# Optimization experiments

Hardware: AMD Instinct MI355X
Metric: run time of the kernel (lower is better)

Reference implementation:

```python
import jax, jax.numpy as jnp
import numpy as np
from jax import lax

B, S, V, E, H, L, LAT = 32, 64, 32000, 128, 512, 2, 64

def setup_inputs() -> dict:
    key = jax.random.key(0)
    ks = jax.random.split(key, 40)
    sc = 0.05
    inputs = jax.random.randint(ks[0], (B, S), 0, V, dtype=jnp.int32)
    lengths = jnp.sort(jax.random.randint(ks[1], (B,), 1, S + 1, dtype=jnp.int32))[::-1]
    lengths = lengths.at[0].set(S)  # enforce_sorted=True, max length == S for static shapes
    d = {
        'inputs': inputs,
        'lengths': lengths,
        'noise': jax.random.normal(ks[2], (L, B, LAT), jnp.float32),
        'embed_table': jax.random.normal(ks[3], (V, E), jnp.float32) * sc,
        'enc_Wm': jax.random.normal(ks[4], (LAT, E), jnp.float32) * sc,
        'enc_bm': jnp.zeros((LAT,), jnp.float32),
        'enc_Wv': jax.random.normal(ks[5], (LAT, E), jnp.float32) * sc,
        'enc_bv': jnp.zeros((LAT,), jnp.float32),
        'W_l2r': jax.random.normal(ks[6], (H, LAT), jnp.float32) * sc,
        'b_l2r': jnp.zeros((H,), jnp.float32),
        'gru_Wih0': jax.random.normal(ks[7], (3 * H, E), jnp.float32) * sc,
        'gru_Whh0': jax.random.normal(ks[8], (3 * H, H), jnp.float32) * sc,
        'gru_bih0': jnp.zeros((3 * H,), jnp.float32),
        'gru_bhh0': jnp.zeros((3 * H,), jnp.float32),
        'gru_Wih1': jax.random.normal(ks[9], (3 * H, H), jnp.float32) * sc,
        'gru_Whh1': jax.random.normal(ks[10], (3 * H, H), jnp.float32) * sc,
        'gru_bih1': jnp.zeros((3 * H,), jnp.float32),
        'gru_bhh1': jnp.zeros((3 * H,), jnp.float32),
        'W_out': jax.random.normal(ks[11], (V, H), jnp.float32) * sc,
        'b_out': jnp.zeros((V,), jnp.float32),
        'logp_W1': jax.random.normal(ks[12], (200, LAT), jnp.float32) * sc,
        'logp_b1': jnp.zeros((200,), jnp.float32),
        'logp_W2': jax.random.normal(ks[13], (100, 200), jnp.float32) * sc,
        'logp_b2': jnp.zeros((100,), jnp.float32),
        'logp_W3': jax.random.normal(ks[14], (1, 100), jnp.float32) * sc,
        'logp_b3': jnp.zeros((1,), jnp.float32),
        'sas_W1': jax.random.normal(ks[15], (200, LAT), jnp.float32) * sc,
        'sas_b1': jnp.zeros((200,), jnp.float32),
        'sas_W2': jax.random.normal(ks[16], (100, 200), jnp.float32) * sc,
        'sas_b2': jnp.zeros((100,), jnp.float32),
        'sas_W3': jax.random.normal(ks[17], (1, 100), jnp.float32) * sc,
        'sas_b3': jnp.zeros((1,), jnp.float32),
    }
    return d

def _gru_layer(x, h0, Wih, Whh, bih, bhh, lengths):
    # x: [B,T,D]; PyTorch GRU gate order: r, z, n. Packed semantics: state frozen
    # and output zero beyond each sample's length.
    T = x.shape[1]
    xW = jnp.einsum('btd,gd->btg', x, Wih) + bih          # [B,T,3H] one big GEMM
    tmask = jnp.arange(T)[:, None] < lengths[None, :]      # [T,B]
    def step(h, inp):
        xw_t, m_t = inp                                    # [B,3H], [B]
        hW = h @ Whh.T + bhh
        xr, xz, xn = jnp.split(xw_t, 3, axis=-1)
        hr, hz, hn = jnp.split(hW, 3, axis=-1)
        r = jax.nn.sigmoid(xr + hr)
        u = jax.nn.sigmoid(xz + hz)
        n = jnp.tanh(xn + r * hn)
        h_new = (1.0 - u) * n + u * h
        m = m_t[:, None]
        h = jnp.where(m, h_new, h)
        out = jnp.where(m, h_new, 0.0)
        return h, out
    hT, outs = lax.scan(step, h0, (xW.transpose(1, 0, 2), tmask))
    return outs.transpose(1, 0, 2), hT                     # [B,T,H], [B,H]

def _mlp3(x, W1, b1, W2, b2, W3, b3):
    h = jax.nn.relu(x @ W1.T + b1)
    h = jax.nn.relu(h @ W2.T + b2)
    return (h @ W3.T + b3).reshape(-1)

def reference(inputs, lengths, noise, embed_table, enc_Wm, enc_bm, enc_Wv, enc_bv,
              W_l2r, b_l2r, gru_Wih0, gru_Whh0, gru_bih0, gru_bhh0,
              gru_Wih1, gru_Whh1, gru_bih1, gru_bhh1, W_out, b_out,
              logp_W1, logp_b1, logp_W2, logp_b2, logp_W3, logp_b3,
              sas_W1, sas_b1, sas_W2, sas_b2, sas_W3, sas_b3):
    emb = embed_table[inputs]                              # [B,S,E] gather
    # ragged masked segment-sum: sum embeddings of tokens with id > 2 per sample
    mask = (inputs > 2)[..., None].astype(emb.dtype)
    vec_frag = jnp.sum(emb * mask, axis=1)                 # [B,E]
    mean = vec_frag @ enc_Wm.T + enc_bm                    # [B,LAT]
    logv = vec_frag @ enc_Wv.T + enc_bv
    std = jnp.exp(0.5 * logv)
    z = noise * std + mean                                 # [L,B,LAT]
    pred_logp = _mlp3(mean, logp_W1, logp_b1, logp_W2, logp_b2, logp_W3, logp_b3)
    pred_sas = _mlp3(mean, sas_W1, sas_b1, sas_W2, sas_b2, sas_W3, sas_b3)
    state = z @ W_l2r.T + b_l2r                            # [L,B,H]
    # decoder: 2-layer GRU (eval mode: no dropout), then vocab projection
    out0, _ = _gru_layer(emb, state[0], gru_Wih0, gru_Whh0, gru_bih0, gru_bhh0, lengths)
    out1, _ = _gru_layer(out0, state[1], gru_Wih1, gru_Whh1, gru_bih1, gru_bhh1, lengths)
    output = out1 @ W_out.T + b_out                        # [B,S,V]
    return (output, mean, std, z, pred_logp, pred_sas)
```

## Files before the change

### kernel.cpp

```cpp
#include <hip/hip_runtime.h>


typedef __attribute__((ext_vector_type(8))) short bf16x8_t;
typedef __attribute__((ext_vector_type(8))) unsigned short u16x8_t;
typedef __attribute__((ext_vector_type(4))) float f32x4_t;
typedef __attribute__((ext_vector_type(8))) _Float16 f16x8_t;
typedef __attribute__((ext_vector_type(4))) unsigned int u32x4_t;

#define AS_AGENT __HIP_MEMORY_SCOPE_AGENT

static __device__ __forceinline__ unsigned short f2bf(float f) {
    unsigned int u = __float_as_uint(f);
    u += 0x7fffu + ((u >> 16) & 1u);
    return (unsigned short)(u >> 16);
}
static __device__ __forceinline__ unsigned short bfround(unsigned int u) {
    u += 0x7fffu + ((u >> 16) & 1u);
    return (unsigned short)(u >> 16);
}
static __device__ __forceinline__ unsigned short f2h(float f) {
    _Float16 h = (_Float16)f;
    return __builtin_bit_cast(unsigned short, h);
}
static __device__ __forceinline__ float sigmoidf_(float x) {
    return 1.f / (1.f + __expf(-x));
}

__global__ __launch_bounds__(256) void embed_encoder_kernel(
    const int* __restrict__ tok, const float* __restrict__ table,
    const float* __restrict__ Wih0f,
    const float* __restrict__ Wm, const float* __restrict__ bm,
    const float* __restrict__ Wv, const float* __restrict__ bv,
    const float* __restrict__ noise,
    const float* __restrict__ Wl2r, const float* __restrict__ bl2r,
    const float* __restrict__ lW1, const float* __restrict__ lb1,
    const float* __restrict__ lW2, const float* __restrict__ lb2,
    const float* __restrict__ lW3, const float* __restrict__ lb3,
    const float* __restrict__ sW1, const float* __restrict__ sb1,
    const float* __restrict__ sW2, const float* __restrict__ sb2,
    const float* __restrict__ sW3, const float* __restrict__ sb3,
    float* __restrict__ o_mean, float* __restrict__ o_std, float* __restrict__ o_z,
    float* __restrict__ o_logp, float* __restrict__ o_sas,
    float* __restrict__ state,
    unsigned short* __restrict__ embb,
    unsigned short* __restrict__ Wih0b)
{
    const int b = blockIdx.x, tid = threadIdx.x;
    __shared__ float v_[128], mn[64], sd[64], zz[2][64], hh1[200], hh2[100];
    if (tid < 128) {
        const int e = tid;
        float acc = 0.f;
        for (int s = 0; s < 64; ++s) {
            int id = tok[b * 64 + s];
            float v = table[(size_t)id * 128 + e];
            embb[(size_t)(b * 64 + s) * 128 + e] = f2bf(v);
            if (id > 2) acc += v;
        }
        v_[e] = acc;
    }
    for (int i = b * 256 + tid; i < 49152; i += 8192) {
        float4 v = reinterpret_cast<const float4*>(Wih0f)[i];
        ushort4 o;
        o.x = f2bf(v.x); o.y = f2bf(v.y); o.z = f2bf(v.z); o.w = f2bf(v.w);
        reinterpret_cast<ushort4*>(Wih0b)[i] = o;
    }
    __syncthreads();
    if (tid < 128) {
        int j = tid & 63;
        bool isv = tid >= 64;
        const float* W = (isv ? Wv : Wm) + j * 128;
        float a = isv ? bv[j] : bm[j];
#pragma unroll 4
        for (int k = 0; k < 128; ++k) a = fmaf(v_[k], W[k], a);
        if (!isv) { mn[j] = a; o_mean[b * 64 + j] = a; }
        else      { float s = __expf(0.5f * a); sd[j] = s; o_std[b * 64 + j] = s; }
    }
    __syncthreads();
    if (tid < 128) {
        int l = tid >> 6, j = tid & 63;
        float zv = fmaf(noise[(l * 32 + b) * 64 + j], sd[j], mn[j]);
        zz[l][j] = zv;
        o_z[(l * 32 + b) * 64 + j] = zv;
    }
    __syncthreads();
#pragma unroll
    for (int p = 0; p < 4; ++p) {
        int tt = p * 256 + tid;
        int l = tt >> 9, hd = tt & 511;
        const float* W = Wl2r + hd * 64;
        float a = bl2r[hd];
#pragma unroll 4
        for (int k = 0; k < 64; ++k) a = fmaf(zz[l][k], W[k], a);
        state[(size_t)(l * 32 + b) * 512 + hd] = a;
    }
    if (tid < 200) {
        const float* W = lW1 + tid * 64;
        float a = lb1[tid];
        for (int k = 0; k < 64; ++k) a = fmaf(mn[k], W[k], a);
        hh1[tid] = fmaxf(a, 0.f);
    }
    __syncthreads();
    if (tid < 100) {
        const float* W = lW2 + tid * 200;
        float a = lb2[tid];
        for (int k = 0; k < 200; ++k) a = fmaf(hh1[k], W[k], a);
        hh2[tid] = fmaxf(a, 0.f);
    }
    __syncthreads();
    if (tid == 0) {
        float a = lb3[0];
        for (int k = 0; k < 100; ++k) a = fmaf(hh2[k], lW3[k], a);
        o_logp[b] = a;
    }
    __syncthreads();
    if (tid < 200) {
        const float* W = sW1 + tid * 64;
        float a = sb1[tid];
        for (int k = 0; k < 64; ++k) a = fmaf(mn[k], W[k], a);
        hh1[tid] = fmaxf(a, 0.f);
    }
    __syncthreads();
    if (tid < 100) {
        const float* W = sW2 + tid * 200;
        float a = sb2[tid];
        for (int k = 0; k < 200; ++k) a = fmaf(hh1[k], W[k], a);
        hh2[tid] = fmaxf(a, 0.f);
    }
    __syncthreads();
    if (tid == 0) {
        float a = sb3[0];
        for (int k = 0; k < 100; ++k) a = fmaf(hh2[k], sW3[k], a);
        o_sas[b] = a;
    }
}

__global__ __launch_bounds__(256) void gemm_bt_kernel(
    const unsigned short* __restrict__ A,
    const unsigned short* __restrict__ B,
    const float* __restrict__ bias,
    float* __restrict__ C,
    int M, int N, int K)
{
    __shared__ unsigned short lA[128 * 64];
    __shared__ unsigned short lB[128 * 64];
    const int tid = threadIdx.x;
    const int lane = tid & 63;
    const int wave = tid >> 6;
    const int wm = wave >> 1, wn = wave & 1;
    const int m0 = blockIdx.y * 128, n0 = blockIdx.x * 128;

    f32x4_t acc[4][4];
#pragma unroll
    for (int i = 0; i < 4; ++i)
#pragma unroll
        for (int j = 0; j < 4; ++j) acc[i][j] = (f32x4_t){0.f, 0.f, 0.f, 0.f};

    for (int kt = 0; kt < K; kt += 64) {
#pragma unroll
        for (int p = 0; p < 4; ++p) {
            int g = p * 256 + tid;
            int row = g >> 3, c8 = g & 7;
            int dst = row * 64 + ((c8 ^ (row & 7)) << 3);
            *(u16x8_t*)&lA[dst] = *(const u16x8_t*)(A + (size_t)(m0 + row) * K + kt + (c8 << 3));
            *(u16x8_t*)&lB[dst] = *(const u16x8_t*)(B + (size_t)(n0 + row) * K + kt + (c8 << 3));
        }
        __syncthreads();
#pragma unroll
        for (int kc = 0; kc < 2; ++kc) {
            bf16x8_t af[4], bfr[4];
            int c8 = kc * 4 + (lane >> 4);
#pragma unroll
            for (int i = 0; i < 4; ++i) {
                int ra = wm * 64 + i * 16 + (lane & 15);
                af[i] = *(const bf16x8_t*)&lA[ra * 64 + ((c8 ^ (ra & 7)) << 3)];
                int rb = wn * 64 + i * 16 + (lane & 15);
                bfr[i] = *(const bf16x8_t*)&lB[rb * 64 + ((c8 ^ (rb & 7)) << 3)];
            }
#pragma unroll
            for (int i = 0; i < 4; ++i)
#pragma unroll
                for (int j = 0; j < 4; ++j)
                    acc[i][j] = __builtin_amdgcn_mfma_f32_16x16x32_bf16(af[i], bfr[j], acc[i][j], 0, 0, 0);
        }
        __syncthreads();
    }
    const int lm = (lane >> 4) * 4, ln = lane & 15;
#pragma unroll
    for (int i = 0; i < 4; ++i) {
        int gm = m0 + wm * 64 + i * 16 + lm;
#pragma unroll
        for (int j = 0; j < 4; ++j) {
            int gn = n0 + wn * 64 + j * 16 + ln;
            float bb = bias ? bias[gn] : 0.f;
#pragma unroll
            for (int r = 0; r < 4; ++r)
                C[(size_t)(gm + r) * N + gn] = acc[i][j][r] + bb;
        }
    }
}

#define NWG_L0 16
#define NWG_TOT 48
#define NWG_ALL 256
#define NWG_GEMM 208
#define OCH 32832

__global__ __launch_bounds__(512) void gru_fused_kernel(
    const float* __restrict__ xW0,
    const float* __restrict__ Whh0, const float* __restrict__ bhh0,
    const float* __restrict__ Whh1, const float* __restrict__ Wih1,
    const float* __restrict__ bih1, const float* __restrict__ bhh1,
    const float* __restrict__ hinit,
    const int* __restrict__ lengths,
    unsigned short* __restrict__ h0x,
    unsigned short* __restrict__ h1x,
    unsigned short* __restrict__ o0x,
    unsigned short* __restrict__ out1x,
    const float* __restrict__ Woutf,
    unsigned short* __restrict__ Woutb,
    const float* __restrict__ bout,
    float* __restrict__ outp,
    int* __restrict__ flags)
{
    __shared__ __align__(16) char smem[157184];
    const int tid = threadIdx.x;
    const int wg = blockIdx.x;
    const int lane = tid & 63;
    const int wave = tid >> 6;
    unsigned int* __restrict__ h0x32 = (unsigned int*)h0x;
    unsigned int* __restrict__ h1x32 = (unsigned int*)h1x;
    unsigned int* __restrict__ o0x32 = (unsigned int*)o0x;
    unsigned int* __restrict__ o1x32 = (unsigned int*)out1x;

    (void)__hip_atomic_load(&flags[0], __ATOMIC_ACQUIRE, AS_AGENT);

    if (wg >= NWG_TOT) {
        unsigned short* lA = (unsigned short*)smem;
        unsigned short* lB = (unsigned short*)(smem + 16384);
        const int g = wg - NWG_TOT;
        const int wm = wave >> 2;
        const int wn = wave & 3;

        for (int pn = g; pn < 250; pn += NWG_GEMM) {
            const u32x4_t* src = (const u32x4_t*)Woutf + (size_t)pn * 16384;
            unsigned long long* dst = (unsigned long long*)Woutb + (size_t)pn * 16384;
            for (int i = tid; i < 16384; i += 512) {
                u32x4_t q = __builtin_nontemporal_load(src + i);
                unsigned int lo = (unsigned int)bfround(q[0]) | ((unsigned int)bfround(q[1]) << 16);
                unsigned int hi = (unsigned int)bfround(q[2]) | ((unsigned int)bfround(q[3]) << 16);
                unsigned long long w = (unsigned long long)lo | ((unsigned long long)hi << 32);
                __hip_atomic_store(dst + i, w, __ATOMIC_RELAXED, AS_AGENT);
            }
            asm volatile("s_waitcnt vmcnt(0)" ::: "memory");
            __syncthreads();
            if (tid == 0)
                __hip_atomic_store(&flags[2048 + pn * 16], 1, __ATOMIC_RELAXED, AS_AGENT);
        }

        int mPrev = -1;
        for (int T = g; T < 4000; T += NWG_GEMM) {
            const int m = T / 250, n = T % 250;
            if (m != mPrev) {
                if (wave == 0) {
                    const int tgt = 4 * m + 6;
                    for (;;) {
                        int v = 0x40000000;
                        if (lane < 32)
                            v = __hip_atomic_load(&flags[(NWG_L0 + lane) << 5],
                                                  __ATOMIC_RELAXED, AS_AGENT);
                        if (__all(v >= tgt)) break;
                        __builtin_amdgcn_s_sleep(8);
                    }
                }
                mPrev = m;
            }
            if (wave == 0) {
                while (__hip_atomic_load(&flags[2048 + n * 16], __ATOMIC_RELAXED, AS_AGENT) < 1)
                    __builtin_amdgcn_s_sleep(8);
            }
            __syncthreads();

            f32x4_t acc[4][2];
#pragma unroll
            for (int i = 0; i < 4; ++i)
#pragma unroll
                for (int j = 0; j < 2; ++j) acc[i][j] = (f32x4_t){0.f, 0.f, 0.f, 0.f};

            for (int kt = 0; kt < 512; kt += 64) {
#pragma unroll
                for (int p = 0; p < 2; ++p) {
                    int gi = p * 512 + tid;
                    int row = gi >> 3, c8 = gi & 7;
                    int dst = row * 64 + ((c8 ^ (row & 7)) << 3);
                    u32x4_t qa = *(const u32x4_t*)(out1x + (size_t)m * 65664 +
                                                   row * 512 + kt + (c8 << 3));
                    u32x4_t qb = *(const u32x4_t*)(Woutb + ((size_t)(n * 128 + row)) * 512 +
                                                   kt + (c8 << 3));
                    *(u32x4_t*)&lA[dst] = qa;
                    *(u32x4_t*)&lB[dst] = qb;
                }
                __syncthreads();
#pragma unroll
                for (int kc = 0; kc < 2; ++kc) {
                    bf16x8_t af[4], bfr[2];
                    int c8 = kc * 4 + (lane >> 4);
#pragma unroll
                    for (int i = 0; i < 4; ++i) {
                        int ra = wm * 64 + i * 16 + (lane & 15);
                        af[i] = *(const bf16x8_t*)&lA[ra * 64 + ((c8 ^ (ra & 7)) << 3)];
                    }
#pragma unroll
                    for (int j = 0; j < 2; ++j) {
                        int rb = wn * 32 + j * 16 + (lane & 15);
                        bfr[j] = *(const bf16x8_t*)&lB[rb * 64 + ((c8 ^ (rb & 7)) << 3)];
                    }
#pragma unroll
                    for (int i = 0; i < 4; ++i)
#pragma unroll
                        for (int j = 0; j < 2; ++j)
                            acc[i][j] = __builtin_amdgcn_mfma_f32_16x16x32_bf16(
                                af[i], bfr[j], acc[i][j], 0, 0, 0);
                }
                __syncthreads();
            }
            const int lm = (lane >> 4) * 4, ln = lane & 15;
#pragma unroll
            for (int i = 0; i < 4; ++i) {
                int rl0 = wm * 64 + i * 16 + lm;
#pragma unroll
                for (int j = 0; j < 2; ++j) {
                    int gn = n * 128 + wn * 32 + j * 16 + ln;
                    float bb = bout[gn];
#pragma unroll
                    for (int r = 0; r < 4; ++r) {
                        int rl = rl0 + r;
                        int t = 4 * m + (rl >> 5), b = rl & 31;
                        __builtin_nontemporal_store(acc[i][j][r] + bb,
                            &outp[(size_t)(b * 64 + t) * 32000 + gn]);
                    }
                }
            }
        }
        return;
    }

    unsigned short* Wl = (unsigned short*)smem;
    u32x4_t* hstage4 = (u32x4_t*)(smem + 98304);
    float* csm = (float*)(smem + 131072);
#define CSM(p, gt, b, c) csm[((((p)*3 + (gt)) * 32 + (b)) * 34) + (c)]
    const int gate = wave >> 1;
    const int mt = wave & 1;

    if (wg < NWG_L0) {
        const int d0 = wg * 32;
        for (int idx = tid; idx < 6144; idx += 512) {
            int ln = idx & 63, kk = (idx >> 6) & 15, nt = (idx >> 10) & 1, g_ = idx >> 11;
            int grow = g_ * 512 + d0 + nt * 16 + (ln & 15);
            int k = kk * 32 + ((ln >> 4) << 3);
            const float* src = Whh0 + (size_t)grow * 512 + k;
            f16x8_t v;
#pragma unroll
            for (int j = 0; j < 8; ++j) v[j] = (_Float16)src[j];
            *(f16x8_t*)&Wl[idx << 3] = v;
        }
        const int ub = tid >> 4, dpl = (tid & 15) * 2, ud = d0 + dpl;
        float h_lo = hinit[(size_t)ub * 512 + ud];
        float h_hi = hinit[(size_t)ub * 512 + ud + 1];
        const float br_lo = bhh0[ud],        br_hi = bhh0[ud + 1];
        const float bz_lo = bhh0[512 + ud],  bz_hi = bhh0[512 + ud + 1];
        const float bn_lo = bhh0[1024 + ud], bn_hi = bhh0[1024 + ud + 1];
        const int lenb = lengths[ub];
        {
            unsigned int hw = (unsigned int)f2h(h_lo) | ((unsigned int)f2h(h_hi) << 16);
            __hip_atomic_store(&h0x32[ub * 256 + (ud >> 1)], hw, __ATOMIC_RELAXED, AS_AGENT);
        }
        asm volatile("s_waitcnt vmcnt(0)" ::: "memory");
        __syncthreads();
        if (tid == 0) __hip_atomic_store(&flags[wg << 5], 1, __ATOMIC_RELAXED, AS_AGENT);
        const float* xrow = xW0 + (size_t)(ub * 64) * 1536 + ud;
        float2 px_r = *(const float2*)(xrow);
        float2 px_z = *(const float2*)(xrow + 512);
        float2 px_n = *(const float2*)(xrow + 1024);

        for (int r = 0; r < 64; ++r) {
            if (wave == 0) {
                for (;;) {
                    int v = 0x40000000;
                    int tgt = (lane < NWG_L0) ? (r + 1) : (r - 2);
                    if (lane < NWG_TOT)
                        v = __hip_atomic_load(&flags[lane << 5], __ATOMIC_RELAXED, AS_AGENT);
                    else
                        tgt = 0;
                    if (__all(v >= tgt)) break;
                    __builtin_amdgcn_s_sleep(1);
                }
            }
            __syncthreads();
            {
                const char* srcb = (const char*)h0x + ((r & 1) << 15);
                u32x4_t q0, q1, q2, q3;
                asm volatile("global_load_dwordx4 %0, %1, off sc0 sc1"
                             : "=v"(q0) : "v"(srcb + ((size_t)tid << 4)) : "memory");
                asm volatile("global_load_dwordx4 %0, %1, off sc0 sc1"
                             : "=v"(q1) : "v"(srcb + ((size_t)(512 + tid) << 4)) : "memory");
                asm volatile("global_load_dwordx4 %0, %1, off sc0 sc1"
                             : "=v"(q2) : "v"(srcb + ((size_t)(1024 + tid) << 4)) : "memory");
                asm volatile("global_load_dwordx4 %0, %1, off sc0 sc1"
                             : "=v"(q3) : "v"(srcb + ((size_t)(1536 + tid) << 4)) : "memory");
                asm volatile("s_waitcnt vmcnt(0)" ::: "memory");
                int g0 = tid, g1 = 512 + tid, g2 = 1024 + tid, g3 = 1536 + tid;
                hstage4[g0 ^ ((g0 >> 6) & 7)] = q0;
                hstage4[g1 ^ ((g1 >> 6) & 7)] = q1;
                hstage4[g2 ^ ((g2 >> 6) & 7)] = q2;
                hstage4[g3 ^ ((g3 >> 6) & 7)] = q3;
            }
            __syncthreads();
            if (wave < 6) {
                const int brow = mt * 16 + (lane & 15);
                const int ko = lane >> 4;
                f32x4_t acc0 = (f32x4_t){0.f, 0.f, 0.f, 0.f};
                f32x4_t acc1 = (f32x4_t){0.f, 0.f, 0.f, 0.f};
#pragma unroll
                for (int kk = 0; kk < 16; ++kk) {
                    int gg = brow * 64 + kk * 4 + ko;
                    f16x8_t af = __builtin_bit_cast(f16x8_t, hstage4[gg ^ (brow & 7)]);
                    f16x8_t bf0 = *(const f16x8_t*)&Wl[(((gate * 2 + 0) * 16 + kk) * 64 + lane) << 3];
                    f16x8_t bf1 = *(const f16x8_t*)&Wl[(((gate * 2 + 1) * 16 + kk) * 64 + lane) << 3];
                    acc0 = __builtin_amdgcn_mfma_f32_16x16x32_f16(af, bf0, acc0, 0, 0, 0);
                    acc1 = __builtin_amdgcn_mfma_f32_16x16x32_f16(af, bf1, acc1, 0, 0, 0);
                }
                const int crow = mt * 16 + ((lane >> 4) << 2), ccol = lane & 15;
#pragma unroll
                for (int rr = 0; rr < 4; ++rr) {
                    CSM(0, gate, crow + rr, ccol) = acc0[rr];
                    CSM(0, gate, crow + rr, 16 + ccol) = acc1[rr];
                }
            }
            __syncthreads();
            unsigned int ow = 0u;
            if (r < lenb) {
                float hr_lo = CSM(0, 0, ub, dpl), hr_hi = CSM(0, 0, ub, dpl + 1);
                float hz_lo = CSM(0, 1, ub, dpl), hz_hi = CSM(0, 1, ub, dpl + 1);
                float hn_lo = CSM(0, 2, ub, dpl), hn_hi = CSM(0, 2, ub, dpl + 1);
                float r0 = sigmoidf_(px_r.x + hr_lo + br_lo);
                float r1 = sigmoidf_(px_r.y + hr_hi + br_hi);
                float u0 = sigmoidf_(px_z.x + hz_lo + bz_lo);
                float u1 = sigmoidf_(px_z.y + hz_hi + bz_hi);
                float n0 = tanhf(px_n.x + r0 * (hn_lo + bn_lo));
                float n1 = tanhf(px_n.y + r1 * (hn_hi + bn_hi));
                h_lo = (1.f - u0) * n0 + u0 * h_lo;
                h_hi = (1.f - u1) * n1 + u1 * h_hi;
                ow = (unsigned int)f2h(h_lo) | ((unsigned int)f2h(h_hi) << 16);
            }
            {
                unsigned int hw = (unsigned int)f2h(h_lo) | ((unsigned int)f2h(h_hi) << 16);
                __hip_atomic_store(&h0x32[((r + 1) & 1) * 8192 + ub * 256 + (ud >> 1)],
                                   hw, __ATOMIC_RELAXED, AS_AGENT);
                __hip_atomic_store(&o0x32[(r & 3) * 8192 + ub * 256 + (ud >> 1)],
                                   ow, __ATOMIC_RELAXED, AS_AGENT);
            }
            asm volatile("s_waitcnt vmcnt(0)" ::: "memory");
            __syncthreads();
            if (tid == 0) __hip_atomic_store(&flags[wg << 5], r + 2, __ATOMIC_RELAXED, AS_AGENT);
            {
                int tn = r + 1 < 64 ? r + 1 : 63;
                const float* xp = xW0 + (size_t)(ub * 64 + tn) * 1536 + ud;
                px_r = *(const float2*)(xp);
                px_z = *(const float2*)(xp + 512);
                px_n = *(const float2*)(xp + 1024);
            }
        }
    } else {
        const int lid = wg - NWG_L0;
        const int d0 = lid * 16;
        for (int idx = tid; idx < 6144; idx += 512) {
            int ln = idx & 63, kk = (idx >> 6) & 31, g_ = idx >> 11;
            int grow = g_ * 512 + d0 + (ln & 15);
            int k = (kk & 15) * 32 + ((ln >> 4) << 3);
            const float* src = (kk < 16 ? Whh1 : Wih1) + (size_t)grow * 512 + k;
            f16x8_t v;
#pragma unroll
            for (int j = 0; j < 8; ++j) v[j] = (_Float16)src[j];
            *(f16x8_t*)&Wl[idx << 3] = v;
        }
        const bool upd = (tid < 256);
        const int ub = tid >> 3, dpl = (tid & 7) * 2, ud = d0 + dpl;
        float h_lo = 0.f, h_hi = 0.f;
        float br_lo = 0.f, br_hi = 0.f, bz_lo = 0.f, bz_hi = 0.f;
        float bxn_lo = 0.f, bxn_hi = 0.f, bhn_lo = 0.f, bhn_hi = 0.f;
        int lenb = 0;
        if (upd) {
            h_lo = hinit[16384 + (size_t)ub * 512 + ud];
            h_hi = hinit[16384 + (size_t)ub * 512 + ud + 1];
            br_lo = bih1[ud] + bhh1[ud];
            br_hi = bih1[ud + 1] + bhh1[ud + 1];
            bz_lo = bih1[512 + ud] + bhh1[512 + ud];
            bz_hi = bih1[512 + ud + 1] + bhh1[512 + ud + 1];
            bxn_lo = bih1[1024 + ud];   bxn_hi = bih1[1024 + ud + 1];
            bhn_lo = bhh1[1024 + ud];   bhn_hi = bhh1[1024 + ud + 1];
            lenb = lengths[ub];
            unsigned int hw = (unsigned int)f2h(h_lo) | ((unsigned int)f2h(h_hi) << 16);
            __hip_atomic_store(&h1x32[8192 + ub * 256 + (ud >> 1)], hw, __ATOMIC_RELAXED, AS_AGENT);
        }
        asm volatile("s_waitcnt vmcnt(0)" ::: "memory");
        __syncthreads();
        if (tid == 0) __hip_atomic_store(&flags[wg << 5], 2, __ATOMIC_RELAXED, AS_AGENT);

        for (int r = 1; r <= 64; ++r) {
            const int t1 = r - 1;
            if (wave == 0) {
                const int tgt = r + 1;
                for (;;) {
                    int v = 0x40000000;
                    if (lane < NWG_TOT)
                        v = __hip_atomic_load(&flags[lane << 5], __ATOMIC_RELAXED, AS_AGENT);
                    if (__all(v >= tgt)) break;
                    __builtin_amdgcn_s_sleep(1);
                }
            }
            __syncthreads();
            u32x4_t a0, a1, a2, a3, b0, b1, b2, b3;
            {
                const char* sh = (const char*)h1x + ((r & 1) << 15);
                const char* so = (const char*)o0x + ((t1 & 3) << 15);
                asm volatile("global_load_dwordx4 %0, %1, off sc0 sc1"
                             : "=v"(a0) : "v"(sh + ((size_t)tid << 4)) : "memory");
                asm volatile("global_load_dwordx4 %0, %1, off sc0 sc1"
                             : "=v"(a1) : "v"(sh + ((size_t)(512 + tid) << 4)) : "memory");
                asm volatile("global_load_dwordx4 %0, %1, off sc0 sc1"
                             : "=v"(a2) : "v"(sh + ((size_t)(1024 + tid) << 4)) : "memory");
                asm volatile("global_load_dwordx4 %0, %1, off sc0 sc1"
                             : "=v"(a3) : "v"(sh + ((size_t)(1536 + tid) << 4)) : "memory");
                asm volatile("global_load_dwordx4 %0, %1, off sc0 sc1"
                             : "=v"(b0) : "v"(so + ((size_t)tid << 4)) : "memory");
                asm volatile("global_load_dwordx4 %0, %1, off sc0 sc1"
                             : "=v"(b1) : "v"(so + ((size_t)(512 + tid) << 4)) : "memory");
                asm volatile("global_load_dwordx4 %0, %1, off sc0 sc1"
                             : "=v"(b2) : "v"(so + ((size_t)(1024 + tid) << 4)) : "memory");
                asm volatile("global_load_dwordx4 %0, %1, off sc0 sc1"
                             : "=v"(b3) : "v"(so + ((size_t)(1536 + tid) << 4)) : "memory");
                asm volatile("s_waitcnt vmcnt(4)" ::: "memory");
                int g0 = tid, g1 = 512 + tid, g2 = 1024 + tid, g3 = 1536 + tid;
                hstage4[g0 ^ ((g0 >> 6) & 7)] = a0;
                hstage4[g1 ^ ((g1 >> 6) & 7)] = a1;
                hstage4[g2 ^ ((g2 >> 6) & 7)] = a2;
                hstage4[g3 ^ ((g3 >> 6) & 7)] = a3;
            }
            __syncthreads();
            f32x4_t acc_h = (f32x4_t){0.f, 0.f, 0.f, 0.f};
            const int brow = mt * 16 + (lane & 15);
            const int ko = lane >> 4;
            if (wave < 6) {
#pragma unroll
                for (int kk = 0; kk < 16; ++kk) {
                    int gg = brow * 64 + kk * 4 + ko;
                    f16x8_t af = __builtin_bit_cast(f16x8_t, hstage4[gg ^ (brow & 7)]);
                    f16x8_t bf = *(const f16x8_t*)&Wl[(((gate * 32 + kk) * 64 + lane)) << 3];
                    acc_h = __builtin_amdgcn_mfma_f32_16x16x32_f16(af, bf, acc_h, 0, 0, 0);
                }
            }
            __syncthreads();
            {
                asm volatile("s_waitcnt vmcnt(0)" ::: "memory");
                int g0 = tid, g1 = 512 + tid, g2 = 1024 + tid, g3 = 1536 + tid;
                hstage4[g0 ^ ((g0 >> 6) & 7)] = b0;
                hstage4[g1 ^ ((g1 >> 6) & 7)] = b1;
                hstage4[g2 ^ ((g2 >> 6) & 7)] = b2;
                hstage4[g3 ^ ((g3 >> 6) & 7)] = b3;
            }
            __syncthreads();
            if (wave < 6) {
                f32x4_t acc_x = (f32x4_t){0.f, 0.f, 0.f, 0.f};
#pragma unroll
                for (int kk = 0; kk < 16; ++kk) {
                    int gg = brow * 64 + kk * 4 + ko;
                    f16x8_t af = __builtin_bit_cast(f16x8_t, hstage4[gg ^ (brow & 7)]);
                    f16x8_t bf = *(const f16x8_t*)&Wl[(((gate * 32 + 16 + kk) * 64 + lane)) << 3];
                    acc_x = __builtin_amdgcn_mfma_f32_16x16x32_f16(af, bf, acc_x, 0, 0, 0);
                }
                const int crow = mt * 16 + ((lane >> 4) << 2), ccol = lane & 15;
#pragma unroll
                for (int rr = 0; rr < 4; ++rr) {
                    CSM(0, gate, crow + rr, ccol) = acc_h[rr];
                    CSM(1, gate, crow + rr, ccol) = acc_x[rr];
                }
            }
            __syncthreads();
            unsigned int ow = 0u;
            if (upd) {
                if (t1 < lenb) {
                    float hr_lo = CSM(0, 0, ub, dpl), hr_hi = CSM(0, 0, ub, dpl + 1);
                    float hz_lo = CSM(0, 1, ub, dpl), hz_hi = CSM(0, 1, ub, dpl + 1);
                    float hn_lo = CSM(0, 2, ub, dpl), hn_hi = CSM(0, 2, ub, dpl + 1);
                    float xr_lo = CSM(1, 0, ub, dpl), xr_hi = CSM(1, 0, ub, dpl + 1);
                    float xz_lo = CSM(1, 1, ub, dpl), xz_hi = CSM(1, 1, ub, dpl + 1);
                    float xn_lo = CSM(1, 2, ub, dpl), xn_hi = CSM(1, 2, ub, dpl + 1);
                    float r0 = sigmoidf_(xr_lo + hr_lo + br_lo);
                    float r1 = sigmoidf_(xr_hi + hr_hi + br_hi);
                    float u0 = sigmoidf_(xz_lo + hz_lo + bz_lo);
                    float u1 = sigmoidf_(xz_hi + hz_hi + bz_hi);
                    float n0 = tanhf(xn_lo + bxn_lo + r0 * (hn_lo + bhn_lo));
                    float n1 = tanhf(xn_hi + bxn_hi + r1 * (hn_hi + bhn_hi));
                    h_lo = (1.f - u0) * n0 + u0 * h_lo;
                    h_hi = (1.f - u1) * n1 + u1 * h_hi;
                    ow = (unsigned int)f2bf(h_lo) | ((unsigned int)f2bf(h_hi) << 16);
                }
                if (r < 64) {
                    unsigned int hw = (unsigned int)f2h(h_lo) | ((unsigned int)f2h(h_hi) << 16);
                    __hip_atomic_store(&h1x32[((r + 1) & 1) * 8192 + ub * 256 + (ud >> 1)],
                                       hw, __ATOMIC_RELAXED, AS_AGENT);
                }
                __hip_atomic_store(&o1x32[(size_t)(t1 >> 2) * OCH +
                                          ((t1 & 3) * 32 + ub) * 256 + (ud >> 1)],
                                   ow, __ATOMIC_RELAXED, AS_AGENT);
            }
            asm volatile("s_waitcnt vmcnt(0)" ::: "memory");
            __syncthreads();
            if (tid == 0)
                __hip_atomic_store(&flags[wg << 5], r + 2, __ATOMIC_RELAXED, AS_AGENT);
        }
    }
#undef CSM
}

extern "C" void kernel_launch(void* const* d_in, const int* in_sizes, int n_in,
                              void* d_out, int out_size, void* d_ws, size_t ws_size,
                              hipStream_t stream) {
    const int*   tok    = (const int*)d_in[0];
    const int*   lens   = (const int*)d_in[1];
    const float* noise  = (const float*)d_in[2];
    const float* table  = (const float*)d_in[3];
    const float* Wm     = (const float*)d_in[4];
    const float* bm_    = (const float*)d_in[5];
    const float* Wv     = (const float*)d_in[6];
    const float* bv_    = (const float*)d_in[7];
    const float* Wl2r   = (const float*)d_in[8];
    const float* bl2r   = (const float*)d_in[9];
    const float* Wih0   = (const float*)d_in[10];
    const float* Whh0   = (const float*)d_in[11];
    const float* bih0   = (const float*)d_in[12];
    const float* bhh0   = (const float*)d_in[13];
    const float* Wih1   = (const float*)d_in[14];
    const float* Whh1   = (const float*)d_in[15];
    const float* bih1   = (const float*)d_in[16];
    const float* bhh1   = (const float*)d_in[17];
    const float* Wout   = (const float*)d_in[18];
    const float* bout   = (const float*)d_in[19];
    const float* lW1 = (const float*)d_in[20]; const float* lb1 = (const float*)d_in[21];
    const float* lW2 = (const float*)d_in[22]; const float* lb2 = (const float*)d_in[23];
    const float* lW3 = (const float*)d_in[24]; const float* lb3 = (const float*)d_in[25];
    const float* sW1 = (const float*)d_in[26]; const float* sb1 = (const float*)d_in[27];
    const float* sW2 = (const float*)d_in[28]; const float* sb2 = (const float*)d_in[29];
    const float* sW3 = (const float*)d_in[30]; const float* sb3 = (const float*)d_in[31];

    float* out    = (float*)d_out;
    float* o_mean = out + 65536000;
    float* o_std  = o_mean + 2048;
    float* o_z    = o_std + 2048;
    float* o_logp = o_z + 4096;
    float* o_sas  = o_logp + 32;

    char* ws = (char*)d_ws;
    unsigned short* Woutb = (unsigned short*)ws;  ws += 32768000;
    unsigned short* Wih0b = (unsigned short*)ws;  ws += 393216;
    unsigned short* embb  = (unsigned short*)ws;  ws += 524288;
    float*          state = (float*)ws;           ws += 131072;
    float*          xW    = (float*)ws;           ws += 12582912;
    unsigned short* out1x = (unsigned short*)ws;  ws += 2101248;
    unsigned short* h0x   = (unsigned short*)ws;  ws += 131072;
    unsigned short* h1x   = (unsigned short*)ws;  ws += 131072;
    unsigned short* o0x   = (unsigned short*)ws;  ws += 262144;
    int*            flgp  = (int*)ws;             ws += 32768;

    (void)hipMemsetAsync(flgp, 0, 32768, stream);

    embed_encoder_kernel<<<dim3(32), dim3(256), 0, stream>>>(
        tok, table, Wih0, Wm, bm_, Wv, bv_, noise, Wl2r, bl2r,
        lW1, lb1, lW2, lb2, lW3, lb3, sW1, sb1, sW2, sb2, sW3, sb3,
        o_mean, o_std, o_z, o_logp, o_sas, state, embb, Wih0b);

    gemm_bt_kernel<<<dim3(12, 16), dim3(256), 0, stream>>>(embb, Wih0b, bih0, xW, 2048, 1536, 128);
    gru_fused_kernel<<<dim3(NWG_ALL), dim3(512), 0, stream>>>(
        xW, Whh0, bhh0, Whh1, Wih1, bih1, bhh1, state, lens,
        h0x, h1x, o0x, out1x, Wout, Woutb, bout, out, flgp);
}
```

Measured before the change: 351.9 us.

## Fuse layer-0 input projection GEMM into persistent GRU kernel with flag sync

Removes the separate gemm_bt_kernel launch and computes the embedding-by-Wih0 projection inside the GEMM workgroups of the fused GRU kernel, writing xW0 with agent-scope stores and publishing per-tile completion flags. The GRU recurrence workgroups spin on these 192 flags before reading xW0. This removes one kernel launch and its serialization gap, and lets the projection overlap with GRU setup such as loading Whh into LDS. The cost is that the GEMM workgroups delay their Wout conversion work, the recurrence now waits on cross-workgroup flags, and the flag buffer doubles in size.

```diff
diff --git a/kernel.cpp b/kernel.cpp
--- a/kernel.cpp
+++ b/kernel.cpp
@@ -134,71 +134,6 @@
     }
 }
 
-__global__ __launch_bounds__(256) void gemm_bt_kernel(
-    const unsigned short* __restrict__ A,
-    const unsigned short* __restrict__ B,
-    const float* __restrict__ bias,
-    float* __restrict__ C,
-    int M, int N, int K)
-{
-    __shared__ unsigned short lA[128 * 64];
-    __shared__ unsigned short lB[128 * 64];
-    const int tid = threadIdx.x;
-    const int lane = tid & 63;
-    const int wave = tid >> 6;
-    const int wm = wave >> 1, wn = wave & 1;
-    const int m0 = blockIdx.y * 128, n0 = blockIdx.x * 128;
-
-    f32x4_t acc[4][4];
-#pragma unroll
-    for (int i = 0; i < 4; ++i)
-#pragma unroll
-        for (int j = 0; j < 4; ++j) acc[i][j] = (f32x4_t){0.f, 0.f, 0.f, 0.f};
-
-    for (int kt = 0; kt < K; kt += 64) {
-#pragma unroll
-        for (int p = 0; p < 4; ++p) {
-            int g = p * 256 + tid;
-            int row = g >> 3, c8 = g & 7;
-            int dst = row * 64 + ((c8 ^ (row & 7)) << 3);
-            *(u16x8_t*)&lA[dst] = *(const u16x8_t*)(A + (size_t)(m0 + row) * K + kt + (c8 << 3));
-            *(u16x8_t*)&lB[dst] = *(const u16x8_t*)(B + (size_t)(n0 + row) * K + kt + (c8 << 3));
-        }
-        __syncthreads();
-#pragma unroll
-        for (int kc = 0; kc < 2; ++kc) {
-            bf16x8_t af[4], bfr[4];
-            int c8 = kc * 4 + (lane >> 4);
-#pragma unroll
-            for (int i = 0; i < 4; ++i) {
-                int ra = wm * 64 + i * 16 + (lane & 15);
-                af[i] = *(const bf16x8_t*)&lA[ra * 64 + ((c8 ^ (ra & 7)) << 3)];
-                int rb = wn * 64 + i * 16 + (lane & 15);
-                bfr[i] = *(const bf16x8_t*)&lB[rb * 64 + ((c8 ^ (rb & 7)) << 3)];
-            }
-#pragma unroll
-            for (int i = 0; i < 4; ++i)
-#pragma unroll
-                for (int j = 0; j < 4; ++j)
-                    acc[i][j] = __builtin_amdgcn_mfma_f32_16x16x32_bf16(af[i], bfr[j], acc[i][j], 0, 0, 0);
-        }
-        __syncthreads();
-    }
-    const int lm = (lane >> 4) * 4, ln = lane & 15;
-#pragma unroll
-    for (int i = 0; i < 4; ++i) {
-        int gm = m0 + wm * 64 + i * 16 + lm;
-#pragma unroll
-        for (int j = 0; j < 4; ++j) {
-            int gn = n0 + wn * 64 + j * 16 + ln;
-            float bb = bias ? bias[gn] : 0.f;
-#pragma unroll
-            for (int r = 0; r < 4; ++r)
-                C[(size_t)(gm + r) * N + gn] = acc[i][j][r] + bb;
-        }
-    }
-}
-
 #define NWG_L0 16
 #define NWG_TOT 48
 #define NWG_ALL 256
@@ -206,7 +141,10 @@
 #define OCH 32832
 
 __global__ __launch_bounds__(512) void gru_fused_kernel(
-    const float* __restrict__ xW0,
+    float* __restrict__ xW0,
+    const unsigned short* __restrict__ embb,
+    const unsigned short* __restrict__ Wih0b,
+    const float* __restrict__ bih0,
     const float* __restrict__ Whh0, const float* __restrict__ bhh0,
     const float* __restrict__ Whh1, const float* __restrict__ Wih1,
     const float* __restrict__ bih1, const float* __restrict__ bhh1,
@@ -241,6 +179,69 @@
         const int wm = wave >> 2;
         const int wn = wave & 3;
 
+        if (g < 192) {
+            const int pm = g / 12, pn = g % 12;
+            f32x4_t pacc[4][2];
+#pragma unroll
+            for (int i = 0; i < 4; ++i)
+#pragma unroll
+                for (int j = 0; j < 2; ++j) pacc[i][j] = (f32x4_t){0.f, 0.f, 0.f, 0.f};
+            for (int kt = 0; kt < 128; kt += 64) {
+#pragma unroll
+                for (int p = 0; p < 2; ++p) {
+                    int gi = p * 512 + tid;
+                    int row = gi >> 3, c8 = gi & 7;
+                    int dst = row * 64 + ((c8 ^ (row & 7)) << 3);
+                    *(u32x4_t*)&lA[dst] = *(const u32x4_t*)(embb +
+                        (size_t)(pm * 128 + row) * 128 + kt + (c8 << 3));
+                    *(u32x4_t*)&lB[dst] = *(const u32x4_t*)(Wih0b +
+                        (size_t)(pn * 128 + row) * 128 + kt + (c8 << 3));
+                }
+                __syncthreads();
+#pragma unroll
+                for (int kc = 0; kc < 2; ++kc) {
+                    int c8 = kc * 4 + (lane >> 4);
+                    bf16x8_t af[4], bfr[2];
+#pragma unroll
+                    for (int i = 0; i < 4; ++i) {
+                        int ra = wm * 64 + i * 16 + (lane & 15);
+                        af[i] = *(const bf16x8_t*)&lA[ra * 64 + ((c8 ^ (ra & 7)) << 3)];
+                    }
+#pragma unroll
+                    for (int j = 0; j < 2; ++j) {
+                        int rb = wn * 32 + j * 16 + (lane & 15);
+                        bfr[j] = *(const bf16x8_t*)&lB[rb * 64 + ((c8 ^ (rb & 7)) << 3)];
+                    }
+#pragma unroll
+                    for (int i = 0; i < 4; ++i)
+#pragma unroll
+                        for (int j = 0; j < 2; ++j)
+                            pacc[i][j] = __builtin_amdgcn_mfma_f32_16x16x32_bf16(
+                                af[i], bfr[j], pacc[i][j], 0, 0, 0);
+                }
+                __syncthreads();
+            }
+            const int lm = (lane >> 4) * 4, ln = lane & 15;
+#pragma unroll
+            for (int i = 0; i < 4; ++i) {
+#pragma unroll
+                for (int j = 0; j < 2; ++j) {
+                    int gn = pn * 128 + wn * 32 + j * 16 + ln;
+                    float bb_ = bih0[gn];
+#pragma unroll
+                    for (int r = 0; r < 4; ++r) {
+                        int gm = pm * 128 + wm * 64 + i * 16 + lm + r;
+                        __hip_atomic_store(&xW0[(size_t)gm * 1536 + gn],
+                                           pacc[i][j][r] + bb_, __ATOMIC_RELAXED, AS_AGENT);
+                    }
+                }
+            }
+            asm volatile("s_waitcnt vmcnt(0)" ::: "memory");
+            __syncthreads();
+            if (tid == 0)
+                __hip_atomic_store(&flags[8192 + g * 16], 1, __ATOMIC_RELAXED, AS_AGENT);
+        }
+
         for (int pn = g; pn < 250; pn += NWG_GEMM) {
             const u32x4_t* src = (const u32x4_t*)Woutf + (size_t)pn * 16384;
             unsigned long long* dst = (unsigned long long*)Woutb + (size_t)pn * 16384;
@@ -377,6 +378,25 @@
         asm volatile("s_waitcnt vmcnt(0)" ::: "memory");
         __syncthreads();
         if (tid == 0) __hip_atomic_store(&flags[wg << 5], 1, __ATOMIC_RELAXED, AS_AGENT);
+
+        if (wave == 0) {
+            for (;;) {
+                int mnv = 1;
+#pragma unroll
+                for (int bb = 0; bb < 3; ++bb) {
+                    int idx = bb * 64 + lane;
+                    if (idx < 192) {
+                        int v = __hip_atomic_load(&flags[8192 + idx * 16],
+                                                  __ATOMIC_RELAXED, AS_AGENT);
+                        mnv = v < mnv ? v : mnv;
+                    }
+                }
+                if (__all(mnv >= 1)) break;
+                __builtin_amdgcn_s_sleep(2);
+            }
+        }
+        __syncthreads();
+
         const float* xrow = xW0 + (size_t)(ub * 64) * 1536 + ud;
         float2 px_r = *(const float2*)(xrow);
         float2 px_z = *(const float2*)(xrow + 512);
@@ -670,17 +690,16 @@
     unsigned short* h0x   = (unsigned short*)ws;  ws += 131072;
     unsigned short* h1x   = (unsigned short*)ws;  ws += 131072;
     unsigned short* o0x   = (unsigned short*)ws;  ws += 262144;
-    int*            flgp  = (int*)ws;             ws += 32768;
-
-    (void)hipMemsetAsync(flgp, 0, 32768, stream);
+    int*            flgp  = (int*)ws;             ws += 65536;
+
+    (void)hipMemsetAsync(flgp, 0, 65536, stream);
 
     embed_encoder_kernel<<<dim3(32), dim3(256), 0, stream>>>(
         tok, table, Wih0, Wm, bm_, Wv, bv_, noise, Wl2r, bl2r,
         lW1, lb1, lW2, lb2, lW3, lb3, sW1, sb1, sW2, sb2, sW3, sb3,
         o_mean, o_std, o_z, o_logp, o_sas, state, embb, Wih0b);
 
-    gemm_bt_kernel<<<dim3(12, 16), dim3(256), 0, stream>>>(embb, Wih0b, bih0, xW, 2048, 1536, 128);
     gru_fused_kernel<<<dim3(NWG_ALL), dim3(512), 0, stream>>>(
-        xW, Whh0, bhh0, Whh1, Wih1, bih1, bhh1, state, lens,
+        xW, embb, Wih0b, bih0, Whh0, bhh0, Whh1, Wih1, bih1, bhh1, state, lens,
         h0x, h1x, o0x, out1x, Wout, Woutb, bout, out, flgp);
 }
```

Measured after the change: 347.3 us (median of 2 runs). No clear change (-1.3%).
